# Performance work log

Measured on AMD Instinct MI355X. Metric: run time of the kernel, lower is better.

Reference implementation:

```python
import jax, jax.numpy as jnp
import numpy as np

N = 8192        # n_nodes == in_features (forced by elementwise input * W)
F_OUT = 128     # out_features
ALPHA = 0.2     # LeakyReLU negative slope
NEG_BIG = -9.0e15


def setup_inputs() -> dict:
    key = jax.random.key(0)
    k1, k2, k3, k4, k5 = jax.random.split(key, 5)
    x = jax.random.normal(k1, (N, F_OUT), dtype=jnp.float32)
    adj = jax.random.randint(k2, (N, N), 0, 2, dtype=jnp.int32)
    # xavier_uniform-style params
    W = jax.random.uniform(k3, (N, F_OUT), dtype=jnp.float32, minval=-1.0, maxval=1.0) * np.float32(1.414 * np.sqrt(6.0 / (N + F_OUT)))
    a = jax.random.uniform(k4, (2 * F_OUT, 1), dtype=jnp.float32, minval=-1.0, maxval=1.0) * np.float32(1.414 * np.sqrt(6.0 / (2 * F_OUT + 1)))
    W2 = jax.random.uniform(k5, (N, 1), dtype=jnp.float32, minval=-1.0, maxval=1.0) * np.float32(1.414 * np.sqrt(6.0 / (N + 1)))
    return {"x": x, "adj": adj, "W": W, "a": a, "W2": W2}


def reference(x, adj, W, a, W2):
    # h = input * W  (elementwise, shapes [N, F])
    h = x * W
    f = W.shape[1]
    # e[i,j] = leakyrelu( concat(h[i], h[j]) @ a ) = leakyrelu(h[i]@a1 + h[j]@a2)
    f1 = h @ a[:f]        # [N, 1]
    f2 = h @ a[f:]        # [N, 1]
    e = jax.nn.leaky_relu(f1 + f2.T, negative_slope=ALPHA)  # [N, N]
    e = jnp.where(adj > 0, e, NEG_BIG)
    attention = jax.nn.softmax(e, axis=1)  # dropout rate = 0.0 -> no-op
    h_prime = attention @ h                # [N, F] (stored as side effect in original)
    # output path: elu( (adj @ W2).T @ x ).T  -> [F, 1]
    adj_f = adj.astype(x.dtype)
    h_prime_3 = ((adj_f @ W2).T @ x).T     # [F, 1]
    out = jax.nn.elu(h_prime_3)            # concat=True branch
    return out, h_prime
```

## Files before the change

kernel.cpp:

```cpp
#include <hip/hip_runtime.h>
#include <hip/hip_bf16.h>

#define ALPHA 0.2f

typedef __attribute__((ext_vector_type(8)))  __bf16 bf16x8;
typedef int          i32x4 __attribute__((ext_vector_type(4)));
typedef float        f32x4 __attribute__((ext_vector_type(4)));
typedef unsigned int u32x4 __attribute__((ext_vector_type(4)));

static __device__ __forceinline__ unsigned short bf16bits(float v) {
    __bf16 b = (__bf16)v;
    unsigned short u;
    __builtin_memcpy(&u, &b, 2);
    return u;
}

__global__ __launch_bounds__(256) void gat_prep(
    const float* __restrict__ x, const float* __restrict__ W, const float* __restrict__ a,
    float* __restrict__ f1, float* __restrict__ f2, unsigned short* __restrict__ hB,
    float* __restrict__ ws_acc)
{
    __shared__ unsigned short lh[32][136];
    int t = threadIdx.x;
    int i0 = blockIdx.x * 32;
    if (blockIdx.x == 0 && t < 128) ws_acc[t] = 0.0f;

    int row = t >> 3, q = t & 7;
    int i = i0 + row;
    const float4* xp  = (const float4*)(x + (size_t)i * 128 + q * 16);
    const float4* wp  = (const float4*)(W + (size_t)i * 128 + q * 16);
    const float4* a1p = (const float4*)(a + q * 16);
    const float4* a2p = (const float4*)(a + 128 + q * 16);
    float p1 = 0.f, p2 = 0.f;
    #pragma unroll
    for (int jj = 0; jj < 4; ++jj) {
        float4 xv = xp[jj], wv = wp[jj], a1v = a1p[jj], a2v = a2p[jj];
        float h0 = xv.x * wv.x, h1 = xv.y * wv.y, h2 = xv.z * wv.z, h3 = xv.w * wv.w;
        p1 += h0 * a1v.x + h1 * a1v.y + h2 * a1v.z + h3 * a1v.w;
        p2 += h0 * a2v.x + h1 * a2v.y + h2 * a2v.z + h3 * a2v.w;
        int fb = q * 16 + jj * 4;
        lh[row][fb + 0] = bf16bits(h0);
        lh[row][fb + 1] = bf16bits(h1);
        lh[row][fb + 2] = bf16bits(h2);
        lh[row][fb + 3] = bf16bits(h3);
    }
    p1 += __shfl_xor(p1, 1); p1 += __shfl_xor(p1, 2); p1 += __shfl_xor(p1, 4);
    p2 += __shfl_xor(p2, 1); p2 += __shfl_xor(p2, 2); p2 += __shfl_xor(p2, 4);
    if (q == 0) { f1[i] = p1; f2[i] = p2; }
    __syncthreads();

    int ftl = t >> 5, s0 = t & 31;
    size_t fragbase = ((size_t)blockIdx.x * 8 + ftl) * 512;
    #pragma unroll
    for (int hw = 0; hw < 2; ++hw) {
        int s = s0 + hw * 32;
        int jl = (s >> 4) * 8;
        int f = ftl * 16 + (s & 15);
        unsigned int p[4];
        #pragma unroll
        for (int k = 0; k < 4; ++k) {
            unsigned int lo = lh[jl + 2 * k][f];
            unsigned int hi = lh[jl + 2 * k + 1][f];
            p[k] = lo | (hi << 16);
        }
        u32x4 v = {p[0], p[1], p[2], p[3]};
        *(u32x4*)(hB + fragbase + s * 8) = v;
    }
}

__global__ __launch_bounds__(256, 2) void gat_main(
    const int* __restrict__ adj, const float* __restrict__ x,
    const float* __restrict__ W2, const float* __restrict__ f1g,
    const float* __restrict__ f2g, const unsigned short* __restrict__ hB,
    float* __restrict__ hp, float* __restrict__ ws_acc)
{
    __shared__ unsigned short tile[4][16][264];
    __shared__ float den_s[4][16], rs_s[4][16];

    int tid = threadIdx.x;
    int w = tid >> 6, l = tid & 63;
    int i0 = blockIdx.x * 16;

    float f1r[16];
    #pragma unroll
    for (int r = 0; r < 16; ++r) f1r[r] = f1g[i0 + r];

    float den[16], rs[16];
    #pragma unroll
    for (int r = 0; r < 16; ++r) { den[r] = 0.f; rs[r] = 0.f; }
    f32x4 acc[8] = {};

    const int jbase0 = w * 2048;
    const int* arow = adj + (size_t)i0 * 8192 + jbase0 + l * 4;
    const float* f2p = f2g + jbase0 + l * 4;
    const float* w2p = W2 + jbase0 + l * 4;

    i32x4 adjreg[16];
    f32x4 f2v, w2v;
    auto issue = [&](int c) {
        int jo = c * 256;
        f2v = *(const f32x4*)(f2p + jo);
        w2v = *(const f32x4*)(w2p + jo);
        #pragma unroll
        for (int r = 0; r < 16; ++r)
            adjreg[r] = __builtin_nontemporal_load(
                (const i32x4*)(arow + (size_t)r * 8192 + jo));
    };
    issue(0);

    const unsigned short* hBw = hB + (size_t)w * 262144 + l * 8;
    const unsigned short* ap  = &tile[w][l & 15][(l >> 4) * 8];

    for (int c = 0; c < 8; ++c) {
        #pragma unroll
        for (int r = 0; r < 16; ++r) {
            i32x4 ad = adjreg[r];
            float g[4];
            float dsum = 0.f, rsum = 0.f;
            #pragma unroll
            for (int e = 0; e < 4; ++e) {
                float tt = f1r[r] + f2v[e];
                float lr = fmaxf(tt, ALPHA * tt);
                float ex = __expf(lr);
                float gg = (ad[e] != 0) ? ex : 0.0f;
                g[e] = gg;
                dsum += gg;
                rsum += (ad[e] != 0) ? w2v[e] : 0.0f;
            }
            den[r] += dsum;
            rs[r] += rsum;
            unsigned int p0 = bf16bits(g[0]) | ((unsigned int)bf16bits(g[1]) << 16);
            unsigned int p1 = bf16bits(g[2]) | ((unsigned int)bf16bits(g[3]) << 16);
            *(uint2*)&tile[w][r][l * 4] = make_uint2(p0, p1);
        }
        if (c < 7) issue(c + 1);

        const unsigned short* bp = hBw + (size_t)c * 32768;
        bf16x8 bbuf[2][8];
        #pragma unroll
        for (int ft = 0; ft < 8; ++ft)
            bbuf[0][ft] = *(const bf16x8*)(bp + ft * 512);
        #pragma unroll
        for (int ksl = 0; ksl < 8; ++ksl) {
            int cur = ksl & 1;
            if (ksl < 7) {
                const unsigned short* bk = bp + (size_t)(ksl + 1) * 4096;
                #pragma unroll
                for (int ft = 0; ft < 8; ++ft)
                    bbuf[cur ^ 1][ft] = *(const bf16x8*)(bk + ft * 512);
            }
            bf16x8 af = *(const bf16x8*)(ap + ksl * 32);
            #pragma unroll
            for (int ft = 0; ft < 8; ++ft)
                acc[ft] = __builtin_amdgcn_mfma_f32_16x16x32_bf16(af, bbuf[cur][ft], acc[ft], 0, 0, 0);
        }
    }

    #pragma unroll
    for (int r = 0; r < 16; ++r) {
        float d = den[r], rr = rs[r];
        #pragma unroll
        for (int off = 1; off < 64; off <<= 1) {
            d += __shfl_xor(d, off);
            rr += __shfl_xor(rr, off);
        }
        if (l == 0) { den_s[w][r] = d; rs_s[w][r] = rr; }
    }

    __syncthreads();

    float* av = (float*)acc;
    if (w != 0) {
        float* dst = (float*)&tile[0][0][0] + (size_t)(w - 1) * 2048;
        #pragma unroll
        for (int j = 0; j < 32; ++j) dst[j * 64 + l] = av[j];
    }
    __syncthreads();

    if (w == 0) {
        #pragma unroll
        for (int ww = 0; ww < 3; ++ww) {
            const float* srcp = (const float*)&tile[0][0][0] + (size_t)ww * 2048;
            #pragma unroll
            for (int j = 0; j < 32; ++j) av[j] += srcp[j * 64 + l];
        }
        int q = l >> 4, col = l & 15;
        float inv[4];
        #pragma unroll
        for (int reg = 0; reg < 4; ++reg) {
            int row = q * 4 + reg;
            float dsum = den_s[0][row] + den_s[1][row] + den_s[2][row] + den_s[3][row];
            inv[reg] = (dsum != 0.f) ? 1.0f / dsum : 0.f;
        }
        #pragma unroll
        for (int ft = 0; ft < 8; ++ft) {
            #pragma unroll
            for (int reg = 0; reg < 4; ++reg) {
                int row = q * 4 + reg;
                __builtin_nontemporal_store(acc[ft][reg] * inv[reg],
                    hp + (size_t)(i0 + row) * 128 + ft * 16 + col);
            }
        }
    } else if (w == 1) {
        float px = 0.f, py = 0.f;
        #pragma unroll
        for (int r = 0; r < 16; ++r) {
            float rm = rs_s[0][r] + rs_s[1][r] + rs_s[2][r] + rs_s[3][r];
            const float* xr = x + (size_t)(i0 + r) * 128;
            px += rm * xr[l];
            py += rm * xr[l + 64];
        }
        atomicAdd(ws_acc + l, px);
        atomicAdd(ws_acc + l + 64, py);
    }
}

__global__ __launch_bounds__(128) void gat_finish(const float* __restrict__ ws_acc,
                                                  float* __restrict__ out)
{
    int t = threadIdx.x;
    float v = ws_acc[t];
    out[t] = (v > 0.f) ? v : (__expf(v) - 1.0f);
}

extern "C" void kernel_launch(void* const* d_in, const int* in_sizes, int n_in,
                              void* d_out, int out_size, void* d_ws, size_t ws_size,
                              hipStream_t stream) {
    const float* x   = (const float*)d_in[0];
    const int*   adj = (const int*)d_in[1];
    const float* W   = (const float*)d_in[2];
    const float* a   = (const float*)d_in[3];
    const float* W2  = (const float*)d_in[4];
    float* out = (float*)d_out;

    float* wsf    = (float*)d_ws;
    float* ws_acc = wsf;
    float* f1     = wsf + 128;
    float* f2     = wsf + 128 + 8192;
    unsigned short* hB = (unsigned short*)(wsf + 128 + 2 * 8192);

    gat_prep<<<256, 256, 0, stream>>>(x, W, a, f1, f2, hB, ws_acc);
    gat_main<<<512, 256, 0, stream>>>(adj, x, W2, f1, f2, hB, out + 128, ws_acc);
    gat_finish<<<1, 128, 0, stream>>>(ws_acc, out);
}
```

Baseline: 388.4 us.

## Split attention K-dimension across two blocks and add separate normalization kernel

Each row-group of 16 rows is now processed by two blocks, each covering half of the neighbor columns. This doubles the grid to 1024 blocks and raises the launch-bounds occupancy hint from 2 to 4. The partial unnormalized h_prime and partial denominators go to workspace, and a new gat_norm kernel sums the two halves and divides. The aim is more parallelism and better latency hiding on the 256-CU device, paid for with extra partial-result traffic and one more kernel launch.

```diff
diff --git a/kernel.cpp b/kernel.cpp
--- a/kernel.cpp
+++ b/kernel.cpp
@@ -68,18 +68,20 @@
     }
 }
 
-__global__ __launch_bounds__(256, 2) void gat_main(
+__global__ __launch_bounds__(256, 4) void gat_main(
     const int* __restrict__ adj, const float* __restrict__ x,
     const float* __restrict__ W2, const float* __restrict__ f1g,
     const float* __restrict__ f2g, const unsigned short* __restrict__ hB,
-    float* __restrict__ hp, float* __restrict__ ws_acc)
+    float* __restrict__ hp_part, float* __restrict__ den_part,
+    float* __restrict__ ws_acc)
 {
     __shared__ unsigned short tile[4][16][264];
     __shared__ float den_s[4][16], rs_s[4][16];
 
     int tid = threadIdx.x;
     int w = tid >> 6, l = tid & 63;
-    int i0 = blockIdx.x * 16;
+    int gid = blockIdx.x >> 1, jh = blockIdx.x & 1;
+    int i0 = gid * 16;
 
     float f1r[16];
     #pragma unroll
@@ -90,7 +92,7 @@
     for (int r = 0; r < 16; ++r) { den[r] = 0.f; rs[r] = 0.f; }
     f32x4 acc[8] = {};
 
-    const int jbase0 = w * 2048;
+    const int jbase0 = jh * 4096 + w * 1024;
     const int* arow = adj + (size_t)i0 * 8192 + jbase0 + l * 4;
     const float* f2p = f2g + jbase0 + l * 4;
     const float* w2p = W2 + jbase0 + l * 4;
@@ -108,10 +110,10 @@
     };
     issue(0);
 
-    const unsigned short* hBw = hB + (size_t)w * 262144 + l * 8;
+    const unsigned short* hBw = hB + (size_t)jbase0 * 128 + l * 8;
     const unsigned short* ap  = &tile[w][l & 15][(l >> 4) * 8];
 
-    for (int c = 0; c < 8; ++c) {
+    for (int c = 0; c < 4; ++c) {
         #pragma unroll
         for (int r = 0; r < 16; ++r) {
             i32x4 ad = adjreg[r];
@@ -133,7 +135,7 @@
             unsigned int p1 = bf16bits(g[2]) | ((unsigned int)bf16bits(g[3]) << 16);
             *(uint2*)&tile[w][r][l * 4] = make_uint2(p0, p1);
         }
-        if (c < 7) issue(c + 1);
+        if (c < 3) issue(c + 1);
 
         const unsigned short* bp = hBw + (size_t)c * 32768;
         bf16x8 bbuf[2][8];
@@ -185,21 +187,19 @@
             for (int j = 0; j < 32; ++j) av[j] += srcp[j * 64 + l];
         }
         int q = l >> 4, col = l & 15;
-        float inv[4];
-        #pragma unroll
-        for (int reg = 0; reg < 4; ++reg) {
-            int row = q * 4 + reg;
-            float dsum = den_s[0][row] + den_s[1][row] + den_s[2][row] + den_s[3][row];
-            inv[reg] = (dsum != 0.f) ? 1.0f / dsum : 0.f;
-        }
+        float* hpb = hp_part + ((size_t)jh * 8192 + i0) * 128;
         #pragma unroll
         for (int ft = 0; ft < 8; ++ft) {
             #pragma unroll
             for (int reg = 0; reg < 4; ++reg) {
                 int row = q * 4 + reg;
-                __builtin_nontemporal_store(acc[ft][reg] * inv[reg],
-                    hp + (size_t)(i0 + row) * 128 + ft * 16 + col);
+                __builtin_nontemporal_store(acc[ft][reg],
+                    hpb + (size_t)row * 128 + ft * 16 + col);
             }
+        }
+        if (l < 16) {
+            float dsum = den_s[0][l] + den_s[1][l] + den_s[2][l] + den_s[3][l];
+            den_part[(size_t)jh * 8192 + i0 + l] = dsum;
         }
     } else if (w == 1) {
         float px = 0.f, py = 0.f;
@@ -212,6 +212,25 @@
         }
         atomicAdd(ws_acc + l, px);
         atomicAdd(ws_acc + l + 64, py);
+    }
+}
+
+__global__ __launch_bounds__(256) void gat_norm(
+    const float* __restrict__ hp_part, const float* __restrict__ den_part,
+    float* __restrict__ hp)
+{
+    int t = threadIdx.x;
+    int row = blockIdx.x * 32 + (t >> 3);
+    int f0 = (t & 7) * 16;
+    float d = den_part[row] + den_part[8192 + row];
+    float inv = (d != 0.f) ? 1.0f / d : 0.f;
+    const f32x4* p0 = (const f32x4*)(hp_part + (size_t)row * 128 + f0);
+    const f32x4* p1 = (const f32x4*)(hp_part + (size_t)(8192 + row) * 128 + f0);
+    f32x4* o = (f32x4*)(hp + (size_t)row * 128 + f0);
+    #pragma unroll
+    for (int k = 0; k < 4; ++k) {
+        f32x4 v = (p0[k] + p1[k]);
+        o[k] = v * inv;
     }
 }
 
@@ -233,13 +252,16 @@
     const float* W2  = (const float*)d_in[4];
     float* out = (float*)d_out;
 
-    float* wsf    = (float*)d_ws;
-    float* ws_acc = wsf;
-    float* f1     = wsf + 128;
-    float* f2     = wsf + 128 + 8192;
+    float* wsf     = (float*)d_ws;
+    float* ws_acc  = wsf;
+    float* f1      = wsf + 128;
+    float* f2      = wsf + 128 + 8192;
     unsigned short* hB = (unsigned short*)(wsf + 128 + 2 * 8192);
+    float* hp_part = wsf + 128 + 2 * 8192 + 524288;
+    float* den_part = hp_part + 2 * 8192 * 128;
 
     gat_prep<<<256, 256, 0, stream>>>(x, W, a, f1, f2, hB, ws_acc);
-    gat_main<<<512, 256, 0, stream>>>(adj, x, W2, f1, f2, hB, out + 128, ws_acc);
+    gat_main<<<1024, 256, 0, stream>>>(adj, x, W2, f1, f2, hB, hp_part, den_part, ws_acc);
+    gat_norm<<<256, 256, 0, stream>>>(hp_part, den_part, out + 128);
     gat_finish<<<1, 128, 0, stream>>>(ws_acc, out);
 }
```

Measured after the change: 583.1 us. 1.5x slower.
